# Kernel tuning notes

Hardware: AMD Instinct MI355X
Metric: run time of the kernel (lower is better)

## Reference

```python
import jax, jax.numpy as jnp
import numpy as np
from jax import lax

# Static config (matches init_kwargs / electrode montage)
B, T, V = 16, 1536, 64
F1, D, H = 16, 2, 4
F2 = F1 * D              # 32
FO = F2 // H             # 8, GAT per-head out dim
K1, K3 = 32, 16          # conv kernel sizes (temporal)
P1, P2 = 8, 4            # avg pool sizes
KNN = 4
EPS = 1e-5
NEG_SLOPE = 0.2          # PyG GATConv leaky_relu slope


def _build_edges():
    # deterministic electrode geometry -> kNN graph, plus PyG self-loops
    rng = np.random.RandomState(0)
    pos = rng.randn(V, 3)
    dmat = np.linalg.norm(pos[:, None] - pos[None, :], axis=-1)
    order = np.argsort(dmat, axis=1)
    nbrs = order[:, 1:KNN + 1]                      # exclude self
    src = np.repeat(np.arange(V), KNN)
    dst = nbrs.reshape(-1)
    # add self loops (GATConv default add_self_loops=True)
    src = np.concatenate([src, np.arange(V)])
    dst = np.concatenate([dst, np.arange(V)])
    return jnp.asarray(np.stack([src, dst]), dtype=jnp.int32)  # (2, E)


def _bn(x, g, b, m, v, axis):
    shp = [1] * x.ndim
    shp[axis] = -1
    rs = lambda a: a.reshape(shp)
    return rs(g) * (x - rs(m)) * lax.rsqrt(rs(v) + EPS) + rs(b)


def _conv_same_t(x, w, k):
    # Conv2d(..., (1,k), padding='same'): torch pads (k-1)//2 left, rest right
    lp = (k - 1) // 2
    return lax.conv_general_dilated(x, w, (1, 1), [(0, 0), (lp, k - 1 - lp)],
                                    dimension_numbers=('NCHW', 'OIHW', 'NCHW'))


def _gat(x, W, a_src, a_dst, bias, src, dst):
    # Batched PyG GATConv (eval mode, dropout off), concat heads.
    # x: (Ng, V, F1); W: (F1, H*FO); a_src/a_dst: (H, FO); bias: (H*FO,)
    Ng = x.shape[0]
    h = jnp.einsum('nvf,fho->nvho', x, W.reshape(F1, H, FO))   # (Ng,V,H,FO)
    es = jnp.einsum('nvho,ho->nvh', h, a_src)[:, src]          # (Ng,E,H)
    ed = jnp.einsum('nvho,ho->nvh', h, a_dst)[:, dst]
    e = jax.nn.leaky_relu(es + ed, NEG_SLOPE)
    # softmax over incoming edges of each target node (segment softmax)
    m = jnp.full((Ng, V, H), -1e30, e.dtype).at[:, dst].max(e)
    ex = jnp.exp(e - m[:, dst])
    den = jnp.zeros((Ng, V, H), e.dtype).at[:, dst].add(ex)
    alpha = ex / den[:, dst]                                   # (Ng,E,H)
    out = jnp.zeros((Ng, V, H, FO), e.dtype).at[:, dst].add(alpha[..., None] * h[:, src])
    return out.reshape(Ng, V, H * FO) + bias


def setup_inputs() -> dict:
    key = jax.random.key(0)
    ks = jax.random.split(key, 16)
    bn = lambda k, c: (1.0 + 0.1 * jax.random.normal(jax.random.fold_in(k, 0), (c,)),
                       0.1 * jax.random.normal(jax.random.fold_in(k, 1), (c,)),
                       0.1 * jax.random.normal(jax.random.fold_in(k, 2), (c,)),
                       0.5 + jax.random.uniform(jax.random.fold_in(k, 3), (c,)))
    bn1 = bn(ks[1], F1); bn2 = bn(ks[2], F2); bn3 = bn(ks[3], F2)
    inp = {
        'x': jax.random.normal(ks[0], (B, 1, V, T), jnp.float32),
        'conv1_w': 0.1 * jax.random.normal(ks[4], (F1, 1, 1, K1), jnp.float32),
        'bn1_g': bn1[0], 'bn1_b': bn1[1], 'bn1_m': bn1[2], 'bn1_v': bn1[3],
        'gat_w': (1.0 / np.sqrt(F1)) * jax.random.normal(ks[5], (F1, H * FO), jnp.float32),
        'gat_asrc': 0.3 * jax.random.normal(ks[6], (H, FO), jnp.float32),
        'gat_adst': 0.3 * jax.random.normal(ks[7], (H, FO), jnp.float32),
        'gat_bias': 0.05 * jax.random.normal(ks[8], (H * FO,), jnp.float32),
        'bn2_g': bn2[0], 'bn2_b': bn2[1], 'bn2_m': bn2[2], 'bn2_v': bn2[3],
        'conv3_w': 0.1 * jax.random.normal(ks[9], (F2, F2, 1, K3), jnp.float32),
        'bn3_g': bn3[0], 'bn3_b': bn3[1], 'bn3_m': bn3[2], 'bn3_v': bn3[3],
        'edge_index': _build_edges(),
    }
    return inp


def reference(x, conv1_w, bn1_g, bn1_b, bn1_m, bn1_v,
              gat_w, gat_asrc, gat_adst, gat_bias,
              bn2_g, bn2_b, bn2_m, bn2_v,
              conv3_w, bn3_g, bn3_b, bn3_m, bn3_v, edge_index):
    src, dst = edge_index[0], edge_index[1]
    # block1: temporal conv + BN
    h = _conv_same_t(x, conv1_w, K1)                 # (B,F1,V,T)
    h = _bn(h, bn1_g, bn1_b, bn1_m, bn1_v, 1)
    # spatial GNN over B*T independent electrode graphs
    xg = h.transpose(0, 3, 2, 1).reshape(B * T, V, F1)
    g = _gat(xg, gat_w, gat_asrc, gat_adst, gat_bias, src, dst)   # (BT,V,F2)
    g = g.mean(axis=1).reshape(B, T, F2).transpose(0, 2, 1)       # (B,F2,T)
    g = _bn(g, bn2_g, bn2_b, bn2_m, bn2_v, 1)[:, :, None, :]      # (B,F2,1,T)
    # tail: elu -> pool -> conv -> bn -> elu -> pool (dropout = eval no-op)
    h = jax.nn.elu(g)
    h = h.reshape(B, F2, 1, T // P1, P1).mean(-1)
    h = _conv_same_t(h, conv3_w, K3)
    h = _bn(h, bn3_g, bn3_b, bn3_m, bn3_v, 1)
    h = jax.nn.elu(h)
    h = h.reshape(B, F2, 1, T // P1 // P2, P2).mean(-1)           # (B,F2,1,48)
    return h
```

## Files before the change

### kernel.cpp

```cpp
#include <hip/hip_runtime.h>
#include <math.h>

#define TPB 256

constexpr int Bc = 16, Tc = 1536;
constexpr int T2c = 192;
constexpr float EPSc = 1e-5f;
constexpr float NSLOPE = 0.2f;
constexpr int MDI = 16;
constexpr int MDO = 8;

constexpr int OW_WEFF = 0;
constexpr int OW_CHL  = 1024;
constexpr int OW_A2   = 1056;
constexpr int OW_C2   = 1088;
constexpr int OW_WES  = 1184;
constexpr int OW_CES  = 1440;
constexpr int OW_GRAPH= 1448;
constexpr int OW_P    = 1872;

constexpr int GB_INTS = 417;

constexpr int L_XT  = 0;
constexpr int L_WF  = 2624;
constexpr int L_WE  = 3648;
constexpr int L_WB  = 3904;
constexpr int L_Y   = 5984;
constexpr int L_G   = 7296;
constexpr int L_CHL = 7552;
constexpr int L_GR  = 7584;
constexpr int L_TOT = 8001;

__global__ void prep_kernel(const float* __restrict__ c1w,
                            const float* __restrict__ g1, const float* __restrict__ b1,
                            const float* __restrict__ m1, const float* __restrict__ v1,
                            const float* __restrict__ W,  const float* __restrict__ bias,
                            const float* __restrict__ asrc, const float* __restrict__ adst,
                            const float* __restrict__ g2, const float* __restrict__ b2,
                            const float* __restrict__ m2, const float* __restrict__ v2,
                            const int* __restrict__ ei, int ne, float* __restrict__ ws)
{
    const int tid = threadIdx.x;
    __shared__ float sweff[1024];
    __shared__ float schl[32];
    __shared__ int isrcp_i[64 * MDI];
    __shared__ int outdst_i[64 * MDO];
    __shared__ int inslot[64], outslot[64];

    for (int idx = tid; idx < 1024; idx += TPB) {
        int k = idx >> 5, f2 = idx & 31;
        float s = 0.f;
        for (int f = 0; f < 16; f++) {
            float a1 = g1[f] * rsqrtf(v1[f] + EPSc);
            s += a1 * W[f * 32 + f2] * c1w[f * 32 + k];
        }
        ws[OW_WEFF + idx] = s;
        sweff[idx] = s;
    }
    for (int f2 = tid; f2 < 32; f2 += TPB) {
        float s = 0.f;
        for (int f = 0; f < 16; f++) {
            float a1 = g1[f] * rsqrtf(v1[f] + EPSc);
            float c1 = b1[f] - a1 * m1[f];
            s += c1 * W[f * 32 + f2];
        }
        ws[OW_CHL + f2] = s;
        schl[f2] = s;
        float a2 = g2[f2] * rsqrtf(v2[f2] + EPSc);
        ws[OW_A2 + f2] = a2;
        ws[OW_C2 + f2] = b2[f2] + a2 * (bias[f2] - m2[f2]);
    }

    for (int i = tid; i < 64 * MDI; i += TPB) isrcp_i[i] = 0;
    for (int i = tid; i < 64 * MDO; i += TPB) outdst_i[i] = 0;
    if (tid < 64) { inslot[tid] = 0; outslot[tid] = 0; }
    __syncthreads();
    for (int e = tid; e < ne; e += TPB) {
        int s = ei[e], d = ei[ne + e];
        int pi = atomicAdd(&inslot[d], 1);
        if (pi < MDI) isrcp_i[d * MDI + pi] = s;
        int po = atomicAdd(&outslot[s], 1);
        if (po < MDO) outdst_i[s * MDO + po] = d;
    }
    __syncthreads();
    if (tid < 128) {
        int k = tid >> 2, h = tid & 3;
        float s1 = 0.f, s2 = 0.f;
        for (int o = 0; o < 8; o++) {
            float wv = sweff[k * 32 + h * 8 + o];
            s1 = fmaf(asrc[h * 8 + o], wv, s1);
            s2 = fmaf(adst[h * 8 + o], wv, s2);
        }
        ws[OW_WES + tid] = s1;
        ws[OW_WES + 128 + tid] = s2;
    }
    if (tid < 4) {
        float s1 = 0.f, s2 = 0.f;
        for (int o = 0; o < 8; o++) {
            float cv = schl[tid * 8 + o];
            s1 = fmaf(asrc[tid * 8 + o], cv, s1);
            s2 = fmaf(adst[tid * 8 + o], cv, s2);
        }
        ws[OW_CES + tid] = s1;
        ws[OW_CES + 4 + tid] = s2;
    }
    unsigned char* gb = (unsigned char*)(ws + OW_GRAPH);
    for (int i = tid; i < 64 * MDI; i += TPB) gb[i] = (unsigned char)isrcp_i[i];
    for (int i = tid; i < 64 * MDO; i += TPB) gb[1088 + i] = (unsigned char)outdst_i[i];
    if (tid < 64) {
        gb[1024 + tid] = (unsigned char)(inslot[tid] < MDI ? inslot[tid] : MDI);
        gb[1600 + tid] = (unsigned char)(outslot[tid] < MDO ? outslot[tid] : MDO);
    }
    __syncthreads();
    if (tid == 0) {
        int mi = 0, mo = 0;
        for (int d = 0; d < 64; d++) {
            int a = gb[1024 + d], o = gb[1600 + d];
            mi = a > mi ? a : mi;
            mo = o > mo ? o : mo;
        }
        gb[1664] = (unsigned char)mi;
        gb[1665] = (unsigned char)mo;
    }
}

__global__ __launch_bounds__(TPB, 5) void gat_kernel(const float* __restrict__ x,
                                                     const float* __restrict__ wfp,
                                                     const float* __restrict__ chlp,
                                                     const float* __restrict__ wesed,
                                                     const float* __restrict__ cesed,
                                                     const float* __restrict__ a2p,
                                                     const float* __restrict__ c2p,
                                                     const int* __restrict__ graphi,
                                                     float* __restrict__ pout)
{
    __shared__ __align__(16) float sm[L_TOT];

    const int tid  = threadIdx.x;
    const int b    = blockIdx.x / 192;
    const int tile = blockIdx.x % 192;
    const int t0   = tile * 8;

    for (int idx = tid; idx < 64 * 41; idx += TPB) {
        int v = idx / 41, j = idx % 41;
        float val = 0.f;
        if (j < 39) {
            int t = t0 - 15 + j;
            val = (t >= 0 && t < Tc) ? x[(b * 64 + v) * Tc + t] : 0.f;
        } else if (j == 39) val = 1.0f;
        sm[L_XT + idx] = val;
    }
    for (int idx = tid; idx < 1024; idx += TPB) sm[L_WF + idx] = wfp[idx];
    sm[L_WE + tid] = wesed[tid];
    if (tid < 32) sm[L_CHL + tid] = chlp[tid];
    {
        int* gd = (int*)&sm[L_GR];
        for (int idx = tid; idx < GB_INTS; idx += TPB) gd[idx] = graphi[idx];
    }
    __syncthreads();

    const int h = tid >> 6, v = tid & 63;
    const unsigned char* gb = (const unsigned char*)&sm[L_GR];

    float aes[8], aed[8];
    {
        const float cesh = cesed[h], cedh = cesed[4 + h];
        const float* xrow = &sm[L_XT + v * 41];
        #pragma unroll
        for (int t = 0; t < 8; t++) { aes[t] = cesh; aed[t] = cedh; }
        float xr[8];
        #pragma unroll
        for (int q = 0; q < 7; q++) xr[q] = xrow[q];
        #pragma unroll
        for (int k = 0; k < 32; k++) {
            xr[(k + 7) & 7] = xrow[k + 7];
            const float wek = sm[L_WE + k * 4 + h];
            const float wdk = sm[L_WE + 128 + k * 4 + h];
            #pragma unroll
            for (int t = 0; t < 8; t++) {
                const float xv = xr[(k + t) & 7];
                aes[t] = fmaf(xv, wek, aes[t]);
                aed[t] = fmaf(xv, wdk, aed[t]);
            }
        }
    }

    {
        const int indeg = gb[1024 + v];
        const int mdin  = gb[1664];
        float den[8] = { 0.f,0.f,0.f,0.f,0.f,0.f,0.f,0.f };
        for (int e = 0; e < mdin; e++) {
            const int s = gb[v * MDI + e];
            const float valid = (e < indeg) ? 1.f : 0.f;
            #pragma unroll
            for (int t = 0; t < 8; t++) {
                float ev = __shfl(aes[t], s) + aed[t];
                ev = ev > 0.f ? ev : NSLOPE * ev;
                den[t] += valid * __expf(ev);
            }
        }
        float rden[8];
        #pragma unroll
        for (int t = 0; t < 8; t++) rden[t] = 1.f / den[t];

        const int odeg = gb[1600 + v];
        const int mdo  = gb[1665];
        float wb[8] = { 0.f,0.f,0.f,0.f,0.f,0.f,0.f,0.f };
        for (int j = 0; j < mdo; j++) {
            const int d = gb[1088 + v * MDO + j];
            const float valid = (j < odeg) ? 1.f : 0.f;
            #pragma unroll
            for (int t = 0; t < 8; t++) {
                float ev = aes[t] + __shfl(aed[t], d);
                ev = ev > 0.f ? ev : NSLOPE * ev;
                wb[t] += valid * __expf(ev) * __shfl(rden[t], d);
            }
        }
        #pragma unroll
        for (int t = 0; t < 8; t++) sm[L_WB + h * 520 + t * 65 + v] = wb[t];
    }
    __asm__ volatile("s_waitcnt lgkmcnt(0)" ::: "memory");

    {
        const int t = v >> 3, cg = v & 7;
        const float* wbrow = &sm[L_WB + h * 520 + t * 65];
        float ya[5] = { 0.f, 0.f, 0.f, 0.f, 0.f };
        for (int vv = 0; vv < 64; vv++) {
            const float wbv = wbrow[vv];
            const float* xv = &sm[L_XT + vv * 41 + cg];
            #pragma unroll
            for (int q = 0; q < 5; q++)
                ya[q] = fmaf(wbv, xv[q * 8], ya[q]);
        }
        float* yrow = &sm[L_Y + h * 328 + t * 41];
        #pragma unroll
        for (int q = 0; q < 5; q++) yrow[cg + q * 8] = ya[q];
    }
    __asm__ volatile("s_waitcnt lgkmcnt(0)" ::: "memory");

    {
        const int t = v >> 3, o = v & 7, f2 = h * 8 + o;
        const float* yrow = &sm[L_Y + h * 328 + t * 41];
        float acc = sm[L_CHL + f2] * yrow[39];
        #pragma unroll
        for (int k = 0; k < 32; k++)
            acc = fmaf(sm[L_WF + k * 32 + f2], yrow[t + k], acc);
        sm[L_G + t * 32 + f2] = acc;
    }
    __syncthreads();

    if (tid < 32) {
        const float a2l = a2p[tid], c2l = c2p[tid];
        float s = 0.f;
        #pragma unroll
        for (int t = 0; t < 8; t++) {
            float gv = sm[L_G + t * 32 + tid] * (1.f / 64.f);
            float y = fmaf(a2l, gv, c2l);
            s += y > 0.f ? y : __expf(y) - 1.f;
        }
        pout[(b * T2c + tile) * 32 + tid] = s * 0.125f;
    }
}

__global__ __launch_bounds__(TPB) void conv3_kernel(const float* __restrict__ pp,
                                                    const float* __restrict__ w3,
                                                    const float* __restrict__ g3,
                                                    const float* __restrict__ b3,
                                                    const float* __restrict__ m3,
                                                    const float* __restrict__ v3,
                                                    float* __restrict__ outp)
{
    __shared__ float w3s[16 * 1057];
    __shared__ float pl[63 * 32];
    __shared__ float q[48 * 32];
    const int tid = threadIdx.x;
    const int b = blockIdx.x >> 2, cc = blockIdx.x & 3;

    for (int idx4 = tid; idx4 < 4096; idx4 += TPB) {
        const float4 w4 = *(const float4*)(w3 + idx4 * 4);
        const int k0 = (idx4 * 4) & 15, f2i = (idx4 >> 2) & 31, f2o = idx4 >> 7;
        const float wq[4] = { w4.x, w4.y, w4.z, w4.w };
        #pragma unroll
        for (int j = 0; j < 4; j++)
            w3s[(k0 + j) * 1057 + f2i * 33 + f2o] = wq[j];
    }
    for (int idx = tid; idx < 63 * 32; idx += TPB) {
        int r = idx >> 5, f2 = idx & 31;
        int tog = cc * 48 - 7 + r;
        pl[idx] = (tog >= 0 && tog < T2c) ? pp[(b * T2c + tog) * 32 + f2] : 0.f;
    }
    __syncthreads();

    const int f2o = tid & 31, grp = tid >> 5;
    const int tb = grp * 6;
    float acc[6] = { 0.f, 0.f, 0.f, 0.f, 0.f, 0.f };
    for (int f2i = 0; f2i < 32; f2i++) {
        float seg[21];
        #pragma unroll
        for (int r = 0; r < 21; r++) seg[r] = pl[(tb + r) * 32 + f2i];
        #pragma unroll
        for (int k = 0; k < 16; k++) {
            float wv = w3s[k * 1057 + f2i * 33 + f2o];
            #pragma unroll
            for (int j = 0; j < 6; j++)
                acc[j] = fmaf(seg[j + k], wv, acc[j]);
        }
    }
    const float a3 = g3[f2o] * rsqrtf(v3[f2o] + EPSc);
    const float c3 = b3[f2o] - a3 * m3[f2o];
    #pragma unroll
    for (int j = 0; j < 6; j++) {
        float y = fmaf(a3, acc[j], c3);
        y = y > 0.f ? y : __expf(y) - 1.f;
        q[(tb + j) * 32 + f2o] = y;
    }
    __syncthreads();
    for (int idx = tid; idx < 12 * 32; idx += TPB) {
        int t4 = idx >> 5, f2 = idx & 31;
        int r0 = t4 * 4;
        float s = q[r0 * 32 + f2] + q[(r0 + 1) * 32 + f2] +
                  q[(r0 + 2) * 32 + f2] + q[(r0 + 3) * 32 + f2];
        outp[(b * 32 + f2) * 48 + cc * 12 + t4] = s * 0.25f;
    }
}

extern "C" void kernel_launch(void* const* d_in, const int* in_sizes, int n_in,
                              void* d_out, int out_size, void* d_ws, size_t ws_size,
                              hipStream_t stream)
{
    const float* x    = (const float*)d_in[0];
    const float* c1w  = (const float*)d_in[1];
    const float* g1   = (const float*)d_in[2];
    const float* b1   = (const float*)d_in[3];
    const float* m1   = (const float*)d_in[4];
    const float* v1   = (const float*)d_in[5];
    const float* W    = (const float*)d_in[6];
    const float* asrc = (const float*)d_in[7];
    const float* adst = (const float*)d_in[8];
    const float* bias = (const float*)d_in[9];
    const float* g2   = (const float*)d_in[10];
    const float* b2   = (const float*)d_in[11];
    const float* m2   = (const float*)d_in[12];
    const float* v2   = (const float*)d_in[13];
    const float* w3   = (const float*)d_in[14];
    const float* g3   = (const float*)d_in[15];
    const float* b3   = (const float*)d_in[16];
    const float* m3   = (const float*)d_in[17];
    const float* v3   = (const float*)d_in[18];
    const int*   ei   = (const int*)d_in[19];
    const int    ne   = in_sizes[19] / 2;

    float* ws = (float*)d_ws;

    prep_kernel<<<1, TPB, 0, stream>>>(c1w, g1, b1, m1, v1, W, bias, asrc, adst,
                                       g2, b2, m2, v2, ei, ne, ws);

    gat_kernel<<<Bc * T2c, TPB, 0, stream>>>(x,
                                             ws + OW_WEFF, ws + OW_CHL,
                                             ws + OW_WES, ws + OW_CES,
                                             ws + OW_A2, ws + OW_C2,
                                             (const int*)(ws + OW_GRAPH),
                                             ws + OW_P);

    conv3_kernel<<<Bc * 4, TPB, 0, stream>>>(ws + OW_P, w3, g3, b3, m3, v3,
                                             (float*)d_out);
}
```

Baseline: 179.2 us.

## Fold prep kernel into GAT kernel and transpose x tile for vectorized aggregation

Removes the single-block prep kernel launch by recomputing the fused conv1/BN1/GAT weights, attention projections and kNN adjacency tables inside every GAT block. The x tile is stored transposed (time-major with padded stride 68) so the neighbour-weighted aggregation can use float4 loads. BN2 constants are also computed inline. This trades one serial launch and its dependency for redundant per-block setup work (global weight reads, shared atomics, extra barriers) across 3072 blocks.

```diff
diff --git a/kernel.cpp b/kernel.cpp
--- a/kernel.cpp
+++ b/kernel.cpp
@@ -10,170 +10,126 @@
 constexpr int MDI = 16;
 constexpr int MDO = 8;
 
-constexpr int OW_WEFF = 0;
-constexpr int OW_CHL  = 1024;
-constexpr int OW_A2   = 1056;
-constexpr int OW_C2   = 1088;
-constexpr int OW_WES  = 1184;
-constexpr int OW_CES  = 1440;
-constexpr int OW_GRAPH= 1448;
-constexpr int OW_P    = 1872;
-
-constexpr int GB_INTS = 417;
-
 constexpr int L_XT  = 0;
-constexpr int L_WF  = 2624;
-constexpr int L_WE  = 3648;
-constexpr int L_WB  = 3904;
-constexpr int L_Y   = 5984;
-constexpr int L_G   = 7296;
-constexpr int L_CHL = 7552;
-constexpr int L_GR  = 7584;
-constexpr int L_TOT = 8001;
-
-__global__ void prep_kernel(const float* __restrict__ c1w,
-                            const float* __restrict__ g1, const float* __restrict__ b1,
-                            const float* __restrict__ m1, const float* __restrict__ v1,
-                            const float* __restrict__ W,  const float* __restrict__ bias,
-                            const float* __restrict__ asrc, const float* __restrict__ adst,
-                            const float* __restrict__ g2, const float* __restrict__ b2,
-                            const float* __restrict__ m2, const float* __restrict__ v2,
-                            const int* __restrict__ ei, int ne, float* __restrict__ ws)
-{
-    const int tid = threadIdx.x;
-    __shared__ float sweff[1024];
-    __shared__ float schl[32];
-    __shared__ int isrcp_i[64 * MDI];
-    __shared__ int outdst_i[64 * MDO];
-    __shared__ int inslot[64], outslot[64];
-
-    for (int idx = tid; idx < 1024; idx += TPB) {
-        int k = idx >> 5, f2 = idx & 31;
-        float s = 0.f;
-        for (int f = 0; f < 16; f++) {
-            float a1 = g1[f] * rsqrtf(v1[f] + EPSc);
-            s += a1 * W[f * 32 + f2] * c1w[f * 32 + k];
-        }
-        ws[OW_WEFF + idx] = s;
-        sweff[idx] = s;
-    }
-    for (int f2 = tid; f2 < 32; f2 += TPB) {
-        float s = 0.f;
-        for (int f = 0; f < 16; f++) {
-            float a1 = g1[f] * rsqrtf(v1[f] + EPSc);
-            float c1 = b1[f] - a1 * m1[f];
-            s += c1 * W[f * 32 + f2];
-        }
-        ws[OW_CHL + f2] = s;
-        schl[f2] = s;
-        float a2 = g2[f2] * rsqrtf(v2[f2] + EPSc);
-        ws[OW_A2 + f2] = a2;
-        ws[OW_C2 + f2] = b2[f2] + a2 * (bias[f2] - m2[f2]);
-    }
-
-    for (int i = tid; i < 64 * MDI; i += TPB) isrcp_i[i] = 0;
-    for (int i = tid; i < 64 * MDO; i += TPB) outdst_i[i] = 0;
-    if (tid < 64) { inslot[tid] = 0; outslot[tid] = 0; }
-    __syncthreads();
-    for (int e = tid; e < ne; e += TPB) {
-        int s = ei[e], d = ei[ne + e];
-        int pi = atomicAdd(&inslot[d], 1);
-        if (pi < MDI) isrcp_i[d * MDI + pi] = s;
-        int po = atomicAdd(&outslot[s], 1);
-        if (po < MDO) outdst_i[s * MDO + po] = d;
-    }
-    __syncthreads();
-    if (tid < 128) {
-        int k = tid >> 2, h = tid & 3;
-        float s1 = 0.f, s2 = 0.f;
-        for (int o = 0; o < 8; o++) {
-            float wv = sweff[k * 32 + h * 8 + o];
-            s1 = fmaf(asrc[h * 8 + o], wv, s1);
-            s2 = fmaf(adst[h * 8 + o], wv, s2);
-        }
-        ws[OW_WES + tid] = s1;
-        ws[OW_WES + 128 + tid] = s2;
-    }
-    if (tid < 4) {
-        float s1 = 0.f, s2 = 0.f;
-        for (int o = 0; o < 8; o++) {
-            float cv = schl[tid * 8 + o];
-            s1 = fmaf(asrc[tid * 8 + o], cv, s1);
-            s2 = fmaf(adst[tid * 8 + o], cv, s2);
-        }
-        ws[OW_CES + tid] = s1;
-        ws[OW_CES + 4 + tid] = s2;
-    }
-    unsigned char* gb = (unsigned char*)(ws + OW_GRAPH);
-    for (int i = tid; i < 64 * MDI; i += TPB) gb[i] = (unsigned char)isrcp_i[i];
-    for (int i = tid; i < 64 * MDO; i += TPB) gb[1088 + i] = (unsigned char)outdst_i[i];
-    if (tid < 64) {
-        gb[1024 + tid] = (unsigned char)(inslot[tid] < MDI ? inslot[tid] : MDI);
-        gb[1600 + tid] = (unsigned char)(outslot[tid] < MDO ? outslot[tid] : MDO);
-    }
-    __syncthreads();
-    if (tid == 0) {
-        int mi = 0, mo = 0;
-        for (int d = 0; d < 64; d++) {
-            int a = gb[1024 + d], o = gb[1600 + d];
-            mi = a > mi ? a : mi;
-            mo = o > mo ? o : mo;
-        }
-        gb[1664] = (unsigned char)mi;
-        gb[1665] = (unsigned char)mo;
-    }
-}
-
-__global__ __launch_bounds__(TPB, 5) void gat_kernel(const float* __restrict__ x,
-                                                     const float* __restrict__ wfp,
-                                                     const float* __restrict__ chlp,
-                                                     const float* __restrict__ wesed,
-                                                     const float* __restrict__ cesed,
-                                                     const float* __restrict__ a2p,
-                                                     const float* __restrict__ c2p,
-                                                     const int* __restrict__ graphi,
-                                                     float* __restrict__ pout)
+constexpr int L_WB  = 2720;
+constexpr int L_Y   = 4896;
+constexpr int L_WF  = 6208;
+constexpr int L_WE  = 7232;
+constexpr int L_CHL = 7488;
+constexpr int L_CES = 7520;
+constexpr int L_GR  = 7528;
+constexpr int L_CNT = 7912;
+constexpr int L_TOT = 8042;
+constexpr int L_G   = L_GR;
+
+__global__ __launch_bounds__(TPB, 5) void gat_kernel(
+    const float* __restrict__ x,
+    const float* __restrict__ c1w,
+    const float* __restrict__ g1, const float* __restrict__ b1,
+    const float* __restrict__ m1, const float* __restrict__ v1,
+    const float* __restrict__ W,
+    const float* __restrict__ asrc, const float* __restrict__ adst,
+    const float* __restrict__ bias,
+    const float* __restrict__ g2, const float* __restrict__ b2,
+    const float* __restrict__ m2, const float* __restrict__ v2,
+    const int* __restrict__ ei, int ne,
+    float* __restrict__ pout)
 {
     __shared__ __align__(16) float sm[L_TOT];
+    int* ci = (int*)&sm[L_CNT];
+    unsigned char* gb = (unsigned char*)&sm[L_GR];
 
     const int tid  = threadIdx.x;
     const int b    = blockIdx.x / 192;
     const int tile = blockIdx.x % 192;
     const int t0   = tile * 8;
 
-    for (int idx = tid; idx < 64 * 41; idx += TPB) {
-        int v = idx / 41, j = idx % 41;
-        float val = 0.f;
+    for (int idx = tid; idx < 384 + 130; idx += TPB) ((int*)&sm[L_GR])[idx] = 0;
+    for (int idx = tid; idx < 2560; idx += TPB) {
+        const int v = idx / 40, j = idx % 40;
+        float val = 1.0f;
         if (j < 39) {
-            int t = t0 - 15 + j;
+            const int t = t0 - 15 + j;
             val = (t >= 0 && t < Tc) ? x[(b * 64 + v) * Tc + t] : 0.f;
-        } else if (j == 39) val = 1.0f;
-        sm[L_XT + idx] = val;
-    }
-    for (int idx = tid; idx < 1024; idx += TPB) sm[L_WF + idx] = wfp[idx];
-    sm[L_WE + tid] = wesed[tid];
-    if (tid < 32) sm[L_CHL + tid] = chlp[tid];
-    {
-        int* gd = (int*)&sm[L_GR];
-        for (int idx = tid; idx < GB_INTS; idx += TPB) gd[idx] = graphi[idx];
+        }
+        sm[L_XT + j * 68 + v] = val;
+    }
+    __syncthreads();
+
+    for (int e = tid; e < ne; e += TPB) {
+        const int s = ei[e], d = ei[ne + e];
+        const int pi = atomicAdd(&ci[d], 1);
+        if (pi < MDI) gb[d * MDI + pi] = (unsigned char)s;
+        const int po = atomicAdd(&ci[64 + s], 1);
+        if (po < MDO) gb[1024 + s * MDO + po] = (unsigned char)d;
+    }
+    {
+        const int f2 = tid & 31, kb = (tid >> 5) * 4;
+        float s0 = 0.f, s1 = 0.f, s2 = 0.f, s3 = 0.f;
+        for (int f = 0; f < 16; f++) {
+            const float a1 = g1[f] * rsqrtf(v1[f] + EPSc);
+            const float pw = a1 * W[f * 32 + f2];
+            const float* c1r = &c1w[f * 32 + kb];
+            s0 = fmaf(pw, c1r[0], s0);
+            s1 = fmaf(pw, c1r[1], s1);
+            s2 = fmaf(pw, c1r[2], s2);
+            s3 = fmaf(pw, c1r[3], s3);
+        }
+        sm[L_WF + (kb + 0) * 32 + f2] = s0;
+        sm[L_WF + (kb + 1) * 32 + f2] = s1;
+        sm[L_WF + (kb + 2) * 32 + f2] = s2;
+        sm[L_WF + (kb + 3) * 32 + f2] = s3;
+    }
+    if (tid < 32) {
+        float s = 0.f;
+        for (int f = 0; f < 16; f++) {
+            const float a1 = g1[f] * rsqrtf(v1[f] + EPSc);
+            s = fmaf(b1[f] - a1 * m1[f], W[f * 32 + tid], s);
+        }
+        sm[L_CHL + tid] = s;
+    }
+    __syncthreads();
+
+    if (tid < 128) {
+        const int k = tid >> 2, hh = tid & 3;
+        float s1 = 0.f, s2 = 0.f;
+        for (int o = 0; o < 8; o++) {
+            const float wv = sm[L_WF + k * 32 + hh * 8 + o];
+            s1 = fmaf(asrc[hh * 8 + o], wv, s1);
+            s2 = fmaf(adst[hh * 8 + o], wv, s2);
+        }
+        sm[L_WE + tid] = s1;
+        sm[L_WE + 128 + tid] = s2;
+    }
+    if (tid < 4) {
+        float s1 = 0.f, s2 = 0.f;
+        for (int o = 0; o < 8; o++) {
+            const float cv = sm[L_CHL + tid * 8 + o];
+            s1 = fmaf(asrc[tid * 8 + o], cv, s1);
+            s2 = fmaf(adst[tid * 8 + o], cv, s2);
+        }
+        sm[L_CES + tid] = s1;
+        sm[L_CES + 4 + tid] = s2;
+    }
+    if (tid < 64) {
+        atomicMax(&ci[128], ci[tid] < MDI ? ci[tid] : MDI);
+        atomicMax(&ci[129], ci[64 + tid] < MDO ? ci[64 + tid] : MDO);
     }
     __syncthreads();
 
     const int h = tid >> 6, v = tid & 63;
-    const unsigned char* gb = (const unsigned char*)&sm[L_GR];
 
     float aes[8], aed[8];
     {
-        const float cesh = cesed[h], cedh = cesed[4 + h];
-        const float* xrow = &sm[L_XT + v * 41];
+        const float cesh = sm[L_CES + h], cedh = sm[L_CES + 4 + h];
         #pragma unroll
         for (int t = 0; t < 8; t++) { aes[t] = cesh; aed[t] = cedh; }
         float xr[8];
         #pragma unroll
-        for (int q = 0; q < 7; q++) xr[q] = xrow[q];
+        for (int q = 0; q < 7; q++) xr[q] = sm[L_XT + q * 68 + v];
         #pragma unroll
         for (int k = 0; k < 32; k++) {
-            xr[(k + 7) & 7] = xrow[k + 7];
+            xr[(k + 7) & 7] = sm[L_XT + (k + 7) * 68 + v];
             const float wek = sm[L_WE + k * 4 + h];
             const float wdk = sm[L_WE + 128 + k * 4 + h];
             #pragma unroll
@@ -186,8 +142,9 @@
     }
 
     {
-        const int indeg = gb[1024 + v];
-        const int mdin  = gb[1664];
+        const int cin = ci[v];
+        const int indeg = cin < MDI ? cin : MDI;
+        const int mdin  = ci[128];
         float den[8] = { 0.f,0.f,0.f,0.f,0.f,0.f,0.f,0.f };
         for (int e = 0; e < mdin; e++) {
             const int s = gb[v * MDI + e];
@@ -203,11 +160,12 @@
         #pragma unroll
         for (int t = 0; t < 8; t++) rden[t] = 1.f / den[t];
 
-        const int odeg = gb[1600 + v];
-        const int mdo  = gb[1665];
+        const int cout = ci[64 + v];
+        const int odeg = cout < MDO ? cout : MDO;
+        const int mdo  = ci[129];
         float wb[8] = { 0.f,0.f,0.f,0.f,0.f,0.f,0.f,0.f };
         for (int j = 0; j < mdo; j++) {
-            const int d = gb[1088 + v * MDO + j];
+            const int d = gb[1024 + v * MDO + j];
             const float valid = (j < odeg) ? 1.f : 0.f;
             #pragma unroll
             for (int t = 0; t < 8; t++) {
@@ -217,45 +175,49 @@
             }
         }
         #pragma unroll
-        for (int t = 0; t < 8; t++) sm[L_WB + h * 520 + t * 65 + v] = wb[t];
+        for (int t = 0; t < 8; t++) sm[L_WB + h * 544 + t * 68 + v] = wb[t];
     }
     __asm__ volatile("s_waitcnt lgkmcnt(0)" ::: "memory");
 
     {
         const int t = v >> 3, cg = v & 7;
-        const float* wbrow = &sm[L_WB + h * 520 + t * 65];
         float ya[5] = { 0.f, 0.f, 0.f, 0.f, 0.f };
-        for (int vv = 0; vv < 64; vv++) {
-            const float wbv = wbrow[vv];
-            const float* xv = &sm[L_XT + vv * 41 + cg];
-            #pragma unroll
-            for (int q = 0; q < 5; q++)
-                ya[q] = fmaf(wbv, xv[q * 8], ya[q]);
-        }
-        float* yrow = &sm[L_Y + h * 328 + t * 41];
-        #pragma unroll
-        for (int q = 0; q < 5; q++) yrow[cg + q * 8] = ya[q];
-    }
-    __asm__ volatile("s_waitcnt lgkmcnt(0)" ::: "memory");
+        const float* wbbase = &sm[L_WB + h * 544 + t * 68];
+        const float* xbase  = &sm[L_XT + cg * 5 * 68];
+        for (int v4 = 0; v4 < 16; v4++) {
+            const float4 w4 = *(const float4*)(wbbase + v4 * 4);
+            #pragma unroll
+            for (int q = 0; q < 5; q++) {
+                const float4 x4 = *(const float4*)(xbase + q * 68 + v4 * 4);
+                ya[q] = fmaf(w4.x, x4.x, fmaf(w4.y, x4.y,
+                        fmaf(w4.z, x4.z, fmaf(w4.w, x4.w, ya[q]))));
+            }
+        }
+        float* yr = &sm[L_Y + h * 328 + t * 41 + cg * 5];
+        #pragma unroll
+        for (int q = 0; q < 5; q++) yr[q] = ya[q];
+    }
+    __syncthreads();
 
     {
         const int t = v >> 3, o = v & 7, f2 = h * 8 + o;
-        const float* yrow = &sm[L_Y + h * 328 + t * 41];
-        float acc = sm[L_CHL + f2] * yrow[39];
+        const float* yr = &sm[L_Y + h * 328 + t * 41];
+        float acc = sm[L_CHL + f2] * yr[39];
         #pragma unroll
         for (int k = 0; k < 32; k++)
-            acc = fmaf(sm[L_WF + k * 32 + f2], yrow[t + k], acc);
+            acc = fmaf(sm[L_WF + k * 32 + f2], yr[t + k], acc);
         sm[L_G + t * 32 + f2] = acc;
     }
     __syncthreads();
 
     if (tid < 32) {
-        const float a2l = a2p[tid], c2l = c2p[tid];
+        const float a2 = g2[tid] * rsqrtf(v2[tid] + EPSc);
+        const float c2 = b2[tid] + a2 * (bias[tid] - m2[tid]);
         float s = 0.f;
         #pragma unroll
         for (int t = 0; t < 8; t++) {
-            float gv = sm[L_G + t * 32 + tid] * (1.f / 64.f);
-            float y = fmaf(a2l, gv, c2l);
+            const float gv = sm[L_G + t * 32 + tid] * (1.f / 64.f);
+            const float y = fmaf(a2, gv, c2);
             s += y > 0.f ? y : __expf(y) - 1.f;
         }
         pout[(b * T2c + tile) * 32 + tid] = s * 0.125f;
@@ -350,18 +312,12 @@
     const int*   ei   = (const int*)d_in[19];
     const int    ne   = in_sizes[19] / 2;
 
-    float* ws = (float*)d_ws;
-
-    prep_kernel<<<1, TPB, 0, stream>>>(c1w, g1, b1, m1, v1, W, bias, asrc, adst,
-                                       g2, b2, m2, v2, ei, ne, ws);
-
-    gat_kernel<<<Bc * T2c, TPB, 0, stream>>>(x,
-                                             ws + OW_WEFF, ws + OW_CHL,
-                                             ws + OW_WES, ws + OW_CES,
-                                             ws + OW_A2, ws + OW_C2,
-                                             (const int*)(ws + OW_GRAPH),
-                                             ws + OW_P);
-
-    conv3_kernel<<<Bc * 4, TPB, 0, stream>>>(ws + OW_P, w3, g3, b3, m3, v3,
+    float* pbuf = (float*)d_ws;
+
+    gat_kernel<<<Bc * T2c, TPB, 0, stream>>>(x, c1w, g1, b1, m1, v1, W,
+                                             asrc, adst, bias, g2, b2, m2, v2,
+                                             ei, ne, pbuf);
+
+    conv3_kernel<<<Bc * 4, TPB, 0, stream>>>(pbuf, w3, g3, b3, m3, v3,
                                              (float*)d_out);
 }
```

Measured after the change: 187.5 us. +4.7%, slower.

## Transpose GAT shared-memory input tile and vectorize aggregation with float4 reads

Applied to the files above, without the earlier changes.

Stores the per-tile input window time-major with padded stride 68, so loads are coalesced and the aggregation matmul can use float4 LDS reads. Attention-score weights are now read per head from global memory through a wave-uniform scalar pointer instead of from shared memory. The second BN fold moves from the prep kernel into the GAT epilogue, and L_G now aliases the graph region. Shared memory use drops slightly, but a wavefront waitcnt is replaced by a full block barrier.

```diff
diff --git a/kernel.cpp b/kernel.cpp
--- a/kernel.cpp
+++ b/kernel.cpp
@@ -12,32 +12,28 @@
 
 constexpr int OW_WEFF = 0;
 constexpr int OW_CHL  = 1024;
-constexpr int OW_A2   = 1056;
-constexpr int OW_C2   = 1088;
-constexpr int OW_WES  = 1184;
-constexpr int OW_CES  = 1440;
-constexpr int OW_GRAPH= 1448;
-constexpr int OW_P    = 1872;
+constexpr int OW_CES  = 1056;
+constexpr int OW_WES  = 1064;
+constexpr int OW_WED  = 1192;
+constexpr int OW_GRAPH= 1320;
+constexpr int OW_P    = 1740;
 
 constexpr int GB_INTS = 417;
 
 constexpr int L_XT  = 0;
-constexpr int L_WF  = 2624;
-constexpr int L_WE  = 3648;
-constexpr int L_WB  = 3904;
-constexpr int L_Y   = 5984;
-constexpr int L_G   = 7296;
-constexpr int L_CHL = 7552;
-constexpr int L_GR  = 7584;
-constexpr int L_TOT = 8001;
+constexpr int L_WB  = 2720;
+constexpr int L_Y   = 4896;
+constexpr int L_WF  = 6208;
+constexpr int L_CHL = 7232;
+constexpr int L_GR  = 7264;
+constexpr int L_TOT = 7681;
+constexpr int L_G   = L_GR;
 
 __global__ void prep_kernel(const float* __restrict__ c1w,
                             const float* __restrict__ g1, const float* __restrict__ b1,
                             const float* __restrict__ m1, const float* __restrict__ v1,
-                            const float* __restrict__ W,  const float* __restrict__ bias,
+                            const float* __restrict__ W,
                             const float* __restrict__ asrc, const float* __restrict__ adst,
-                            const float* __restrict__ g2, const float* __restrict__ b2,
-                            const float* __restrict__ m2, const float* __restrict__ v2,
                             const int* __restrict__ ei, int ne, float* __restrict__ ws)
 {
     const int tid = threadIdx.x;
@@ -61,14 +57,10 @@
         float s = 0.f;
         for (int f = 0; f < 16; f++) {
             float a1 = g1[f] * rsqrtf(v1[f] + EPSc);
-            float c1 = b1[f] - a1 * m1[f];
-            s += c1 * W[f * 32 + f2];
+            s = fmaf(b1[f] - a1 * m1[f], W[f * 32 + f2], s);
         }
         ws[OW_CHL + f2] = s;
         schl[f2] = s;
-        float a2 = g2[f2] * rsqrtf(v2[f2] + EPSc);
-        ws[OW_A2 + f2] = a2;
-        ws[OW_C2 + f2] = b2[f2] + a2 * (bias[f2] - m2[f2]);
     }
 
     for (int i = tid; i < 64 * MDI; i += TPB) isrcp_i[i] = 0;
@@ -83,6 +75,7 @@
         if (po < MDO) outdst_i[s * MDO + po] = d;
     }
     __syncthreads();
+
     if (tid < 128) {
         int k = tid >> 2, h = tid & 3;
         float s1 = 0.f, s2 = 0.f;
@@ -91,8 +84,8 @@
             s1 = fmaf(asrc[h * 8 + o], wv, s1);
             s2 = fmaf(adst[h * 8 + o], wv, s2);
         }
-        ws[OW_WES + tid] = s1;
-        ws[OW_WES + 128 + tid] = s2;
+        ws[OW_WES + h * 32 + k] = s1;
+        ws[OW_WED + h * 32 + k] = s2;
     }
     if (tid < 4) {
         float s1 = 0.f, s2 = 0.f;
@@ -124,58 +117,62 @@
     }
 }
 
-__global__ __launch_bounds__(TPB, 5) void gat_kernel(const float* __restrict__ x,
-                                                     const float* __restrict__ wfp,
-                                                     const float* __restrict__ chlp,
-                                                     const float* __restrict__ wesed,
-                                                     const float* __restrict__ cesed,
-                                                     const float* __restrict__ a2p,
-                                                     const float* __restrict__ c2p,
-                                                     const int* __restrict__ graphi,
-                                                     float* __restrict__ pout)
+__global__ __launch_bounds__(TPB, 5) void gat_kernel(
+    const float* __restrict__ x,
+    const float* __restrict__ wfp,
+    const float* __restrict__ chlp,
+    const float* __restrict__ cesg,
+    const float* __restrict__ wesg,
+    const float* __restrict__ wedg,
+    const float* __restrict__ bias,
+    const float* __restrict__ g2, const float* __restrict__ b2,
+    const float* __restrict__ m2, const float* __restrict__ v2,
+    const int* __restrict__ graphi,
+    float* __restrict__ pout)
 {
     __shared__ __align__(16) float sm[L_TOT];
+    unsigned char* gb = (unsigned char*)&sm[L_GR];
 
     const int tid  = threadIdx.x;
     const int b    = blockIdx.x / 192;
     const int tile = blockIdx.x % 192;
     const int t0   = tile * 8;
 
-    for (int idx = tid; idx < 64 * 41; idx += TPB) {
-        int v = idx / 41, j = idx % 41;
-        float val = 0.f;
+    for (int idx = tid; idx < GB_INTS; idx += TPB) ((int*)&sm[L_GR])[idx] = graphi[idx];
+    {
+        const float4 w4 = ((const float4*)wfp)[tid];
+        *(float4*)&sm[L_WF + tid * 4] = w4;
+    }
+    if (tid < 32) sm[L_CHL + tid] = chlp[tid];
+    for (int idx = tid; idx < 2560; idx += TPB) {
+        const int v = idx & 63, j = idx >> 6;
+        float val = 1.0f;
         if (j < 39) {
-            int t = t0 - 15 + j;
+            const int t = t0 - 15 + j;
             val = (t >= 0 && t < Tc) ? x[(b * 64 + v) * Tc + t] : 0.f;
-        } else if (j == 39) val = 1.0f;
-        sm[L_XT + idx] = val;
-    }
-    for (int idx = tid; idx < 1024; idx += TPB) sm[L_WF + idx] = wfp[idx];
-    sm[L_WE + tid] = wesed[tid];
-    if (tid < 32) sm[L_CHL + tid] = chlp[tid];
-    {
-        int* gd = (int*)&sm[L_GR];
-        for (int idx = tid; idx < GB_INTS; idx += TPB) gd[idx] = graphi[idx];
+        }
+        sm[L_XT + j * 68 + v] = val;
     }
     __syncthreads();
 
     const int h = tid >> 6, v = tid & 63;
-    const unsigned char* gb = (const unsigned char*)&sm[L_GR];
+    const int hs = __builtin_amdgcn_readfirstlane(h);
+    const float* wesh = wesg + hs * 32;
+    const float* wedh = wedg + hs * 32;
 
     float aes[8], aed[8];
     {
-        const float cesh = cesed[h], cedh = cesed[4 + h];
-        const float* xrow = &sm[L_XT + v * 41];
+        const float cesh = cesg[hs], cedh = cesg[4 + hs];
         #pragma unroll
         for (int t = 0; t < 8; t++) { aes[t] = cesh; aed[t] = cedh; }
         float xr[8];
         #pragma unroll
-        for (int q = 0; q < 7; q++) xr[q] = xrow[q];
+        for (int q = 0; q < 7; q++) xr[q] = sm[L_XT + q * 68 + v];
         #pragma unroll
         for (int k = 0; k < 32; k++) {
-            xr[(k + 7) & 7] = xrow[k + 7];
-            const float wek = sm[L_WE + k * 4 + h];
-            const float wdk = sm[L_WE + 128 + k * 4 + h];
+            xr[(k + 7) & 7] = sm[L_XT + (k + 7) * 68 + v];
+            const float wek = wesh[k];
+            const float wdk = wedh[k];
             #pragma unroll
             for (int t = 0; t < 8; t++) {
                 const float xv = xr[(k + t) & 7];
@@ -217,45 +214,49 @@
             }
         }
         #pragma unroll
-        for (int t = 0; t < 8; t++) sm[L_WB + h * 520 + t * 65 + v] = wb[t];
+        for (int t = 0; t < 8; t++) sm[L_WB + h * 544 + t * 68 + v] = wb[t];
     }
     __asm__ volatile("s_waitcnt lgkmcnt(0)" ::: "memory");
 
     {
         const int t = v >> 3, cg = v & 7;
-        const float* wbrow = &sm[L_WB + h * 520 + t * 65];
         float ya[5] = { 0.f, 0.f, 0.f, 0.f, 0.f };
-        for (int vv = 0; vv < 64; vv++) {
-            const float wbv = wbrow[vv];
-            const float* xv = &sm[L_XT + vv * 41 + cg];
-            #pragma unroll
-            for (int q = 0; q < 5; q++)
-                ya[q] = fmaf(wbv, xv[q * 8], ya[q]);
-        }
-        float* yrow = &sm[L_Y + h * 328 + t * 41];
-        #pragma unroll
-        for (int q = 0; q < 5; q++) yrow[cg + q * 8] = ya[q];
-    }
-    __asm__ volatile("s_waitcnt lgkmcnt(0)" ::: "memory");
+        const float* wbbase = &sm[L_WB + h * 544 + t * 68];
+        const float* xbase  = &sm[L_XT + cg * 5 * 68];
+        for (int v4 = 0; v4 < 16; v4++) {
+            const float4 w4 = *(const float4*)(wbbase + v4 * 4);
+            #pragma unroll
+            for (int q = 0; q < 5; q++) {
+                const float4 x4 = *(const float4*)(xbase + q * 68 + v4 * 4);
+                ya[q] = fmaf(w4.x, x4.x, fmaf(w4.y, x4.y,
+                        fmaf(w4.z, x4.z, fmaf(w4.w, x4.w, ya[q]))));
+            }
+        }
+        float* yr = &sm[L_Y + h * 328 + t * 41 + cg * 5];
+        #pragma unroll
+        for (int q = 0; q < 5; q++) yr[q] = ya[q];
+    }
+    __syncthreads();
 
     {
         const int t = v >> 3, o = v & 7, f2 = h * 8 + o;
-        const float* yrow = &sm[L_Y + h * 328 + t * 41];
-        float acc = sm[L_CHL + f2] * yrow[39];
+        const float* yr = &sm[L_Y + h * 328 + t * 41];
+        float acc = sm[L_CHL + f2] * yr[39];
         #pragma unroll
         for (int k = 0; k < 32; k++)
-            acc = fmaf(sm[L_WF + k * 32 + f2], yrow[t + k], acc);
+            acc = fmaf(sm[L_WF + k * 32 + f2], yr[t + k], acc);
         sm[L_G + t * 32 + f2] = acc;
     }
     __syncthreads();
 
     if (tid < 32) {
-        const float a2l = a2p[tid], c2l = c2p[tid];
+        const float a2 = g2[tid] * rsqrtf(v2[tid] + EPSc);
+        const float c2 = b2[tid] + a2 * (bias[tid] - m2[tid]);
         float s = 0.f;
         #pragma unroll
         for (int t = 0; t < 8; t++) {
-            float gv = sm[L_G + t * 32 + tid] * (1.f / 64.f);
-            float y = fmaf(a2l, gv, c2l);
+            const float gv = sm[L_G + t * 32 + tid] * (1.f / 64.f);
+            const float y = fmaf(a2, gv, c2);
             s += y > 0.f ? y : __expf(y) - 1.f;
         }
         pout[(b * T2c + tile) * 32 + tid] = s * 0.125f;
@@ -352,13 +353,14 @@
 
     float* ws = (float*)d_ws;
 
-    prep_kernel<<<1, TPB, 0, stream>>>(c1w, g1, b1, m1, v1, W, bias, asrc, adst,
-                                       g2, b2, m2, v2, ei, ne, ws);
+    prep_kernel<<<1, TPB, 0, stream>>>(c1w, g1, b1, m1, v1, W, asrc, adst,
+                                       ei, ne, ws);
 
     gat_kernel<<<Bc * T2c, TPB, 0, stream>>>(x,
                                              ws + OW_WEFF, ws + OW_CHL,
-                                             ws + OW_WES, ws + OW_CES,
-                                             ws + OW_A2, ws + OW_C2,
+                                             ws + OW_CES,
+                                             ws + OW_WES, ws + OW_WED,
+                                             bias, g2, b2, m2, v2,
                                              (const int*)(ws + OW_GRAPH),
                                              ws + OW_P);
 
```

Result: faster. 171.5 us (-4.3%).
